# Performance work log

Hardware: AMD Instinct MI355X
Metric: run time of the kernel (lower is better)

## Reference

```python
import jax, jax.numpy as jnp
from jax import lax
import numpy as np


def setup_inputs() -> dict:
    key = jax.random.key(0)
    k1, k2, k3, k4, k5 = jax.random.split(key, 5)
    bs, m, v, L, P = 2, 16, 16, 40320, 32
    preds = jax.random.normal(k1, (bs, m, v, L), dtype=jnp.float32)
    target = jax.random.normal(k2, (bs, v, L), dtype=jnp.float32)
    weights = jax.random.uniform(k3, (L,), dtype=jnp.float32)
    scale = jax.random.uniform(k4, (v,), dtype=jnp.float32)
    # binary-ish patch masks over grid points (float, as in the torch buffer)
    masks = (jax.random.uniform(k5, (P, L)) < 0.25).astype(jnp.float32)
    return {"preds": preds, "target": target, "weights": weights,
            "scale": scale, "masks": masks, "beta": 1}


def _energy_score(x, y, m, beta):
    # x: (bs, m, D) ensemble, y: (bs, D) observation
    diff = x - y[:, None, :]
    a = jnp.sqrt(jnp.sum(diff * diff, axis=-1))            # (bs, m)
    score_a = jnp.mean(jnp.sum(a ** beta, axis=-1)) / m
    # pairwise distances via Gram trick (cdist p=2)
    sq = jnp.sum(x * x, axis=-1)                            # (bs, m)
    g = jnp.einsum('bid,bjd->bij', x, x)                    # (bs, m, m)
    d2 = jnp.maximum(sq[:, :, None] + sq[:, None, :] - 2.0 * g, 0.0)
    pos = d2 > 0
    d = jnp.where(pos, jnp.sqrt(jnp.where(pos, d2, 1.0)), 0.0)
    score_b = jnp.mean(jnp.sum(d ** beta, axis=(1, 2))) / (2 * m * (m - 1))
    return score_a - score_b


def reference(preds, target, weights, scale, masks, beta):
    beta = float(beta)
    bs, m, v, L = preds.shape
    # buffer scaling as in forward()
    p = preds * scale[None, None, :, None] * weights        # (bs, m, v, L)
    t = target * scale[None, :, None] * weights             # (bs, v, L)

    def body(acc, mask):
        # rearrange 'bs m v latlon -> bs m (latlon v)'
        x = (p * mask).transpose(0, 1, 3, 2).reshape(bs, m, L * v)
        y = (t * mask).transpose(0, 2, 1).reshape(bs, L * v)
        return acc + _energy_score(x, y, m, beta), None

    total, _ = lax.scan(body, jnp.float32(0.0), masks)
    return total
```

## Files before the change

kernel.cpp:

```cpp
#include <hip/hip_runtime.h>
#include <math.h>

#define BS 2
#define M 16
#define V 16
#define NROWB 136
#define NROWS 272
#define PMASK 32
#define KZ 32
#define KSTEPS 1260
#define NWORK 128

typedef __attribute__((ext_vector_type(8))) short bf16x8;
typedef __attribute__((ext_vector_type(4))) float f32x4;

static __device__ __forceinline__ unsigned short f2bf(float x) {
    unsigned int u = __float_as_uint(x);
    unsigned int r = (u + 0x7FFFu + ((u >> 16) & 1u)) >> 16;
    return (unsigned short)r;
}


static __device__ __forceinline__ void k1_stage(
    const float* __restrict__ preds, float* __restrict__ dst,
    int b, int v0, int l0, int L, int lane, int wave)
{
#pragma unroll
    for (int n = 0; n < 8; ++n) {
        int r0 = wave * 32 + n * 4;
        int grow = b * 256 + (r0 >> 3) * 16 + v0 + (r0 & 7);
        const float* g = preds + (size_t)(grow + (lane >> 4)) * L
                         + l0 + (lane & 15) * 4;
        __builtin_amdgcn_global_load_lds(
            (const __attribute__((address_space(1))) unsigned int*)g,
            (__attribute__((address_space(3))) unsigned int*)(dst + r0 * 64),
            16, 0, 0);
    }
}

template<int W>
static __device__ __forceinline__ void k1_chunk(
    const float (*__restrict__ xs)[64],
    const float* __restrict__ target,
    const float* __restrict__ scale, float wl,
    int b, int lane, int l0, int L, int v0,
    float* __restrict__ acc)
{
    const int base = (W == 0) ? 0 : 34 * W - 16;
    const int npair = (W == 0) ? 18 : 34;
    const int aoff = (W == 0) ? 16 : 0;

#pragma unroll
    for (int vc = 0; vc < 8; ++vc) {
        int v = v0 + vc;
        float sw = scale[v] * wl;
        float x[M];
#pragma unroll
        for (int i = 0; i < M; ++i)
            x[i] = xs[i * 8 + vc][lane] * sw;
        if (W == 0) {
            float y = target[(size_t)(b * V + v) * L + l0 + lane] * sw;
#pragma unroll
            for (int i = 0; i < M; ++i) {
                float d = x[i] - y;
                acc[i] = fmaf(d, d, acc[i]);
            }
        }
        int k = 0;
#pragma unroll
        for (int i = 0; i < M; ++i) {
#pragma unroll
            for (int j = i + 1; j < M; ++j) {
                if (k >= base && k < base + npair) {
                    float d = x[i] - x[j];
                    acc[aoff + k - base] = fmaf(d, d, acc[aoff + k - base]);
                }
                ++k;
            }
        }
    }
}

__global__ __launch_bounds__(256, 2)
void k1_pairsums(const float* __restrict__ preds, const float* __restrict__ target,
                 const float* __restrict__ weights, const float* __restrict__ scale,
                 const float* __restrict__ masks,
                 unsigned short* __restrict__ S, unsigned short* __restrict__ maskbf,
                 int L)
{
    __shared__ float xs[128][64];
    int t = (int)threadIdx.x;
    int lane = t & 63, wave = t >> 6;
    int l0 = (int)blockIdx.x * 64;
    int b = (int)blockIdx.y;

    k1_stage(preds, &xs[0][0], b, 0, l0, L, lane, wave);

    float wl = weights[l0 + lane];
    if (b == 0) {
#pragma unroll
        for (int pp = 0; pp < 8; ++pp) {
            int p = wave * 8 + pp;
            maskbf[(size_t)p * L + l0 + lane] =
                (masks[(size_t)p * L + l0 + lane] != 0.0f) ? (unsigned short)0x3F80
                                                           : (unsigned short)0;
        }
    }

    float acc[34];
#pragma unroll
    for (int r = 0; r < 34; ++r) acc[r] = 0.0f;

    __syncthreads();

    switch (wave) {
        case 0: k1_chunk<0>(xs, target, scale, wl, b, lane, l0, L, 0, acc); break;
        case 1: k1_chunk<1>(xs, target, scale, wl, b, lane, l0, L, 0, acc); break;
        case 2: k1_chunk<2>(xs, target, scale, wl, b, lane, l0, L, 0, acc); break;
        default: k1_chunk<3>(xs, target, scale, wl, b, lane, l0, L, 0, acc); break;
    }

    __syncthreads();
    k1_stage(preds, &xs[0][0], b, 8, l0, L, lane, wave);
    __syncthreads();

    switch (wave) {
        case 0: k1_chunk<0>(xs, target, scale, wl, b, lane, l0, L, 8, acc); break;
        case 1: k1_chunk<1>(xs, target, scale, wl, b, lane, l0, L, 8, acc); break;
        case 2: k1_chunk<2>(xs, target, scale, wl, b, lane, l0, L, 8, acc); break;
        default: k1_chunk<3>(xs, target, scale, wl, b, lane, l0, L, 8, acc); break;
    }

#pragma unroll
    for (int r = 0; r < 34; ++r)
        S[(size_t)(b * NROWB + 34 * wave + r) * L + l0 + lane] = f2bf(acc[r]);
}

__global__ __launch_bounds__(256, 4)
void k2_mfma(const unsigned short* __restrict__ S,
             const unsigned short* __restrict__ maskbf,
             float* __restrict__ D2p, float* __restrict__ out, int L)
{
    if (blockIdx.x == 0 && blockIdx.y == 0 && threadIdx.x == 0)
        out[0] = 0.0f;

    int lane = (int)(threadIdx.x & 63);
    int wave = (int)(threadIdx.x >> 6);
    int mtile = blockIdx.x;
    int z = blockIdx.y;
    int zw = z * 4 + wave;

    const int q = KSTEPS / NWORK;
    const int rem = KSTEPS % NWORK;
    int start = zw * q + (zw < rem ? zw : rem);
    int cnt = q + (zw < rem ? 1 : 0);

    const unsigned short* Arow =
        S + (size_t)(mtile * 16 + (lane & 15)) * L + (lane >> 4) * 8;
    const unsigned short* B0 =
        maskbf + (size_t)(lane & 15) * L + (lane >> 4) * 8;
    const unsigned short* B1 =
        maskbf + (size_t)(16 + (lane & 15)) * L + (lane >> 4) * 8;

    f32x4 acc0 = {0.f, 0.f, 0.f, 0.f};
    f32x4 acc1 = {0.f, 0.f, 0.f, 0.f};

    for (int s = 0; s < cnt; ++s) {
        int k0 = (start + s) * 32;
        bf16x8 a  = *(const bf16x8*)(Arow + k0);
        bf16x8 b0 = *(const bf16x8*)(B0 + k0);
        bf16x8 b1 = *(const bf16x8*)(B1 + k0);
        acc0 = __builtin_amdgcn_mfma_f32_16x16x32_bf16(a, b0, acc0, 0, 0, 0);
        acc1 = __builtin_amdgcn_mfma_f32_16x16x32_bf16(a, b1, acc1, 0, 0, 0);
    }

    __shared__ float red[4][512];
    int c16 = lane & 15;
#pragma unroll
    for (int reg = 0; reg < 4; ++reg) {
        int r16 = (lane >> 4) * 4 + reg;
        red[wave][r16 * 16 + c16]       = acc0[reg];
        red[wave][256 + r16 * 16 + c16] = acc1[reg];
    }
    __syncthreads();
    int t = (int)threadIdx.x;
#pragma unroll
    for (int u = t; u < 512; u += 256) {
        float v = red[0][u] + red[1][u] + red[2][u] + red[3][u];
        D2p[((size_t)z * 17 + mtile) * 512 + u] = v;
    }
}

__global__ __launch_bounds__(256, 2)
void k3_finalize(const float* __restrict__ D2p, const int* __restrict__ beta_p,
                 float* __restrict__ out)
{
    int t = (int)threadIdx.x;
    int e = blockIdx.x * 256 + t;
    int mtile = e >> 9;
    int flat = e & 511;

    float vbuf[KZ];
#pragma unroll
    for (int z = 0; z < KZ; ++z)
        vbuf[z] = D2p[((size_t)z * 17 + mtile) * 512 + flat];

    float a0 = 0.f, a1 = 0.f, a2 = 0.f, a3 = 0.f;
#pragma unroll
    for (int z = 0; z < KZ; z += 4) {
        a0 += vbuf[z + 0]; a1 += vbuf[z + 1];
        a2 += vbuf[z + 2]; a3 += vbuf[z + 3];
    }
    float d2 = fmaxf((a0 + a1) + (a2 + a3), 0.0f);
    float beta = (float)beta_p[0];
    float d = (beta == 1.0f) ? sqrtf(d2) : powf(d2, 0.5f * beta);

    const float wa = 1.0f / (float)(BS * M);
    const float wb = -1.0f / (float)(BS * M * (M - 1));
    int row = mtile * 16 + ((flat >> 4) & 15);
    int local = row % NROWB;
    float sum = ((local < M) ? wa : wb) * d;

    int lane = t & 63, wv = t >> 6;
#pragma unroll
    for (int off = 32; off > 0; off >>= 1)
        sum += __shfl_down(sum, off, 64);
    __shared__ float red[4];
    if (lane == 0) red[wv] = sum;
    __syncthreads();
    if (t == 0)
        atomicAdd(out, red[0] + red[1] + red[2] + red[3]);
}

extern "C" void kernel_launch(void* const* d_in, const int* in_sizes, int n_in,
                              void* d_out, int out_size, void* d_ws, size_t ws_size,
                              hipStream_t stream)
{
    const float* preds   = (const float*)d_in[0];
    const float* target  = (const float*)d_in[1];
    const float* weights = (const float*)d_in[2];
    const float* scale   = (const float*)d_in[3];
    const float* masks   = (const float*)d_in[4];
    const int*   beta    = (const int*)d_in[5];
    float* out = (float*)d_out;

    int L = in_sizes[2];

    unsigned short* S = (unsigned short*)d_ws;
    size_t s_bytes = (size_t)NROWS * (size_t)L * sizeof(unsigned short);
    unsigned short* maskbf = (unsigned short*)((char*)d_ws + ((s_bytes + 255) & ~(size_t)255));
    size_t m_bytes = (size_t)PMASK * (size_t)L * sizeof(unsigned short);
    float* D2p = (float*)((char*)maskbf + ((m_bytes + 255) & ~(size_t)255));

    dim3 g1(L / 64, BS);
    k1_pairsums<<<g1, 256, 0, stream>>>(preds, target, weights, scale, masks,
                                        S, maskbf, L);

    dim3 g2(17, KZ);
    k2_mfma<<<g2, 256, 0, stream>>>(S, maskbf, D2p, out, L);

    k3_finalize<<<(NROWS * PMASK) / 256, 256, 0, stream>>>(D2p, beta, out);
}
```

Before: 159.0 us.

## Double-buffer k1 LDS staging in four v-chunks to overlap loads with compute

The k1 staging of preds is split into four chunks of 4 variables each, ping-ponging between two LDS buffers so the async global_load_lds of the next chunk overlaps the pair-sum computation of the current one. Per-variable scale*weight factors and the scaled target values are precomputed into registers once instead of being reloaded inside the chunk loop. The aim is to hide global load latency and drop a serialized stage/compute phase. In exchange there are more barriers and extra register arrays (sw, ty), which may raise register pressure under the 2-block launch bound.

```diff
diff --git a/kernel.cpp b/kernel.cpp
--- a/kernel.cpp
+++ b/kernel.cpp
@@ -26,11 +26,11 @@
     int b, int v0, int l0, int L, int lane, int wave)
 {
 #pragma unroll
-    for (int n = 0; n < 8; ++n) {
-        int r0 = wave * 32 + n * 4;
-        int grow = b * 256 + (r0 >> 3) * 16 + v0 + (r0 & 7);
-        const float* g = preds + (size_t)(grow + (lane >> 4)) * L
-                         + l0 + (lane & 15) * 4;
+    for (int n = 0; n < 4; ++n) {
+        int r0 = wave * 16 + n * 4;
+        int r = r0 + (lane >> 4);
+        int grow = b * 256 + (r >> 2) * 16 + v0 + (r & 3);
+        const float* g = preds + (size_t)grow * L + l0 + (lane & 15) * 4;
         __builtin_amdgcn_global_load_lds(
             (const __attribute__((address_space(1))) unsigned int*)g,
             (__attribute__((address_space(3))) unsigned int*)(dst + r0 * 64),
@@ -40,26 +40,25 @@
 
 template<int W>
 static __device__ __forceinline__ void k1_chunk(
-    const float (*__restrict__ xs)[64],
-    const float* __restrict__ target,
-    const float* __restrict__ scale, float wl,
-    int b, int lane, int l0, int L, int v0,
-    float* __restrict__ acc)
+    const float* __restrict__ xsb,
+    const float* __restrict__ ty,
+    const float* __restrict__ sw,
+    int v0, int lane, float* __restrict__ acc)
 {
     const int base = (W == 0) ? 0 : 34 * W - 16;
     const int npair = (W == 0) ? 18 : 34;
     const int aoff = (W == 0) ? 16 : 0;
 
 #pragma unroll
-    for (int vc = 0; vc < 8; ++vc) {
-        int v = v0 + vc;
-        float sw = scale[v] * wl;
+    for (int vc = 0; vc < 4; ++vc) {
+        const int v = v0 + vc;
+        float s = sw[v];
         float x[M];
 #pragma unroll
         for (int i = 0; i < M; ++i)
-            x[i] = xs[i * 8 + vc][lane] * sw;
+            x[i] = xsb[(i * 4 + vc) * 64 + lane] * s;
         if (W == 0) {
-            float y = target[(size_t)(b * V + v) * L + l0 + lane] * sw;
+            float y = ty[v];
 #pragma unroll
             for (int i = 0; i < M; ++i) {
                 float d = x[i] - y;
@@ -88,7 +87,7 @@
                  unsigned short* __restrict__ S, unsigned short* __restrict__ maskbf,
                  int L)
 {
-    __shared__ float xs[128][64];
+    __shared__ float xs[2][4096];
     int t = (int)threadIdx.x;
     int lane = t & 63, wave = t >> 6;
     int l0 = (int)blockIdx.x * 64;
@@ -97,6 +96,15 @@
     k1_stage(preds, &xs[0][0], b, 0, l0, L, lane, wave);
 
     float wl = weights[l0 + lane];
+    float sw[V];
+#pragma unroll
+    for (int v = 0; v < V; ++v) sw[v] = scale[v] * wl;
+    float ty[V];
+    if (wave == 0) {
+#pragma unroll
+        for (int v = 0; v < V; ++v)
+            ty[v] = target[(size_t)(b * V + v) * L + l0 + lane] * sw[v];
+    }
     if (b == 0) {
 #pragma unroll
         for (int pp = 0; pp < 8; ++pp) {
@@ -111,24 +119,18 @@
 #pragma unroll
     for (int r = 0; r < 34; ++r) acc[r] = 0.0f;
 
-    __syncthreads();
-
-    switch (wave) {
-        case 0: k1_chunk<0>(xs, target, scale, wl, b, lane, l0, L, 0, acc); break;
-        case 1: k1_chunk<1>(xs, target, scale, wl, b, lane, l0, L, 0, acc); break;
-        case 2: k1_chunk<2>(xs, target, scale, wl, b, lane, l0, L, 0, acc); break;
-        default: k1_chunk<3>(xs, target, scale, wl, b, lane, l0, L, 0, acc); break;
-    }
-
-    __syncthreads();
-    k1_stage(preds, &xs[0][0], b, 8, l0, L, lane, wave);
-    __syncthreads();
-
-    switch (wave) {
-        case 0: k1_chunk<0>(xs, target, scale, wl, b, lane, l0, L, 8, acc); break;
-        case 1: k1_chunk<1>(xs, target, scale, wl, b, lane, l0, L, 8, acc); break;
-        case 2: k1_chunk<2>(xs, target, scale, wl, b, lane, l0, L, 8, acc); break;
-        default: k1_chunk<3>(xs, target, scale, wl, b, lane, l0, L, 8, acc); break;
+#pragma unroll
+    for (int c = 0; c < 4; ++c) {
+        __syncthreads();
+        if (c < 3)
+            k1_stage(preds, &xs[(c + 1) & 1][0], b, (c + 1) * 4, l0, L, lane, wave);
+        const float* xsb = &xs[c & 1][0];
+        switch (wave) {
+            case 0: k1_chunk<0>(xsb, ty, sw, c * 4, lane, acc); break;
+            case 1: k1_chunk<1>(xsb, ty, sw, c * 4, lane, acc); break;
+            case 2: k1_chunk<2>(xsb, ty, sw, c * 4, lane, acc); break;
+            default: k1_chunk<3>(xsb, ty, sw, c * 4, lane, acc); break;
+        }
     }
 
 #pragma unroll
```

New measurement: 155.5 us. -2.2%, faster.
